# Kernel tuning notes

Hardware: AMD Instinct MI355X
Metric: run time of the kernel (lower is better)

Reference implementation:

```python
import jax, jax.numpy as jnp
import numpy as np

N_NODES = 100000
N_EDGES = 3200000


def sage_conv(x, src, dst, Wl, bl, Wr, n_nodes):
    # PyG SAGEConv: out = lin_l(mean_{j in N(i)} x_j) + lin_r(x_i)
    msgs = x[src]                                            # [E, d]
    agg = jax.ops.segment_sum(msgs, dst, num_segments=n_nodes)
    cnt = jax.ops.segment_sum(jnp.ones((src.shape[0],), x.dtype), dst,
                              num_segments=n_nodes)
    mean = agg / jnp.maximum(cnt, 1.0)[:, None]
    return mean @ Wl.T + bl + x @ Wr.T


def setup_inputs() -> dict:
    key = jax.random.key(0)
    ks = jax.random.split(key, 9)
    x = jax.random.normal(ks[0], (N_NODES, 6), dtype=jnp.float32)
    edge_index = jax.random.randint(ks[1], (2, N_EDGES), 0, N_NODES, dtype=jnp.int32)
    def glorot(k, shape):
        fan_in = shape[1]
        return jax.random.normal(k, shape, dtype=jnp.float32) / np.sqrt(fan_in)
    return {
        "x": x,
        "edge_index": edge_index,
        "W1l": glorot(ks[2], (12, 6)), "b1": jnp.zeros((12,), jnp.float32),
        "W1r": glorot(ks[3], (12, 6)),
        "W2l": glorot(ks[4], (24, 12)), "b2": jnp.zeros((24,), jnp.float32),
        "W2r": glorot(ks[5], (24, 12)),
        "W3l": glorot(ks[6], (6, 24)), "b3": jnp.zeros((6,), jnp.float32),
        "W3r": glorot(ks[7], (6, 24)),
    }


def reference(x, edge_index, W1l, b1, W1r, W2l, b2, W2r, W3l, b3, W3r):
    src, dst = edge_index[0], edge_index[1]
    h = jax.nn.relu(sage_conv(x, src, dst, W1l, b1, W1r, N_NODES))
    h = jax.nn.relu(sage_conv(h, src, dst, W2l, b2, W2r, N_NODES))
    z = sage_conv(h, src, dst, W3l, b3, W3r, N_NODES)          # [N, 6] encoding
    return z
```

## Files before the change

### kernel.cpp

```cpp
#include <hip/hip_runtime.h>
#include <hip/hip_fp16.h>


#define BSHIFT 9
#define BMASK  511
#define NBMAX  256
#define PART_EDGES 4096
#define BCAP   18000

#define NTL(p) __builtin_nontemporal_load(p)

__device__ __forceinline__ unsigned h2u(__half2 h) { return *reinterpret_cast<unsigned*>(&h); }
__device__ __forceinline__ __half2 u2h(unsigned u) { return *reinterpret_cast<__half2*>(&u); }

__device__ __forceinline__ __half2 red32(__half2 v) {
    int x;
    x = __builtin_amdgcn_update_dpp(0, (int)h2u(v), 0x128, 0xf, 0xf, true);
    v = __hadd2(v, u2h((unsigned)x));
    x = __builtin_amdgcn_update_dpp(0, (int)h2u(v), 0x124, 0xf, 0xf, true);
    v = __hadd2(v, u2h((unsigned)x));
    x = __builtin_amdgcn_update_dpp(0, (int)h2u(v), 0x122, 0xf, 0xf, true);
    v = __hadd2(v, u2h((unsigned)x));
    x = __builtin_amdgcn_update_dpp(0, (int)h2u(v), 0x121, 0xf, 0xf, true);
    v = __hadd2(v, u2h((unsigned)x));
    v = __hadd2(v, u2h(__shfl_xor(h2u(v), 16, 64)));
    return v;
}

__global__ void init_bcur(int* __restrict__ bcur, int nb) {
    int t = threadIdx.x;
    if (t < nb) bcur[t] = t * BCAP;
}

__global__ void __launch_bounds__(256)
partition_kernel(const int* __restrict__ src, const int* __restrict__ dst,
                 int* __restrict__ bcur, unsigned* __restrict__ pairs,
                 int E, int nb) {
    __shared__ int hcnt[NBMAX];
    __shared__ int hbase[NBMAX];
    __shared__ int lofs[NBMAX];
    __shared__ int ssc[256];
    __shared__ unsigned sorted[PART_EDGES];
    __shared__ int gpos[PART_EDGES];

    int lo = blockIdx.x * PART_EDGES;
    int hi = min(E, lo + PART_EDGES);
    int cnt = hi - lo;
    int t = threadIdx.x;

    for (int i = t; i < NBMAX; i += 256) hcnt[i] = 0;
    __syncthreads();

    int myd[16]; unsigned mys[16];
#pragma unroll
    for (int k = 0; k < 16; k++) {
        int i = lo + t + k * 256;
        if (i < hi) { myd[k] = NTL(dst + i); mys[k] = (unsigned)NTL(src + i); }
        else myd[k] = -1;
    }
#pragma unroll
    for (int k = 0; k < 16; k++)
        if (myd[k] >= 0) atomicAdd(&hcnt[myd[k] >> BSHIFT], 1);
    __syncthreads();

    int c = (t < nb) ? hcnt[t] : 0;
    if (t < nb) hbase[t] = c ? atomicAdd(&bcur[t], c) : 0;
    ssc[t] = c;
    __syncthreads();
    for (int off = 1; off < 256; off <<= 1) {
        int x = (t >= off) ? ssc[t - off] : 0;
        __syncthreads();
        ssc[t] += x;
        __syncthreads();
    }
    if (t < nb) { lofs[t] = ssc[t] - c; hcnt[t] = ssc[t] - c; }
    __syncthreads();

#pragma unroll
    for (int k = 0; k < 16; k++) {
        if (myd[k] >= 0) {
            int d = myd[k];
            int b = d >> BSHIFT;
            int r = atomicAdd(&hcnt[b], 1);
            sorted[r] = (mys[k] << BSHIFT) | (unsigned)(d & BMASK);
            gpos[r] = hbase[b] + (r - lofs[b]);
        }
    }
    __syncthreads();

    for (int i = t; i < cnt; i += 256)
        pairs[gpos[i]] = sorted[i];
}

__global__ void __launch_bounds__(1024)
csr_build(const unsigned* __restrict__ pairs,
          const int* __restrict__ bcur,
          int* __restrict__ deg, int* __restrict__ offsets,
          int* __restrict__ ssrc, int n) {
    __shared__ int ldeg[512];
    __shared__ int lcur[512];
    __shared__ int ssc[512];
    int b = blockIdx.x;
    int base = b * BCAP;
    int cnt = bcur[b] - base;
    int t = threadIdx.x;
    if (t < 512) ldeg[t] = 0;
    __syncthreads();
    for (int i = t; i < cnt; i += 1024)
        atomicAdd(&ldeg[NTL(pairs + base + i) & BMASK], 1);
    __syncthreads();
    if (t < 512) ssc[t] = ldeg[t];
    __syncthreads();
    for (int off = 1; off < 512; off <<= 1) {
        int x = (t >= off && t < 512) ? ssc[t - off] : 0;
        __syncthreads();
        if (t < 512) ssc[t] += x;
        __syncthreads();
    }
    if (t < 512) {
        int excl = ssc[t] - ldeg[t];
        lcur[t] = excl;
        int node = (b << BSHIFT) + t;
        if (node < n) { offsets[node] = base + excl; deg[node] = ldeg[t]; }
    }
    __syncthreads();
    for (int i = t; i < cnt; i += 1024) {
        unsigned p = NTL(pairs + base + i);
        int loc = p & BMASK;
        int pos = atomicAdd(&lcur[loc], 1);
        ssrc[base + pos] = (int)(p >> BSHIFT);
    }
}

__global__ void pack_x(const float* __restrict__ x, __half* __restrict__ xh,
                       __half* __restrict__ h1, int n) {
    int tid = blockIdx.x * blockDim.x + threadIdx.x;
    if (blockIdx.x == 0 && threadIdx.x < 16)
        h1[(size_t)n * 16 + threadIdx.x] = __float2half(0.f);
    if (tid >= n * 8) return;
    int i = tid >> 3, f = tid & 7;
    xh[tid] = __float2half((f < 6) ? x[i * 6 + f] : 0.f);
}

__global__ void __launch_bounds__(256)
sage_layer1(const __half* __restrict__ xh,
            const int* __restrict__ offsets,
            const int* __restrict__ deg,
            const int* __restrict__ ssrc,
            const float* __restrict__ Wl,
            const float* __restrict__ bb,
            const float* __restrict__ Wr,
            __half* __restrict__ h1, int n) {
    __shared__ float sWl[84], sWr[84], sb[12];
    int t = threadIdx.x;
    if (t < 72) { int r = t / 6, c = t % 6; sWl[r * 7 + c] = Wl[t]; sWr[r * 7 + c] = Wr[t]; }
    if (t < 12) sb[t] = bb[t];
    __syncthreads();

    int wid = (blockIdx.x * blockDim.x + threadIdx.x) >> 6;
    int nwaves = (gridDim.x * blockDim.x) >> 6;
    int wl = threadIdx.x & 63;
    int lane = wl & 31;
    int sub = wl >> 5;

    int r = (lane < 12) ? lane : 0;
    float wl_[6], wr_[6];
#pragma unroll
    for (int f = 0; f < 6; f++) { wl_[f] = sWl[r * 7 + f]; wr_[f] = sWr[r * 7 + f]; }
    float bias = sb[r];

    int npairs = (n + 1) >> 1;
    __half2 z2 = __float2half2_rn(0.f);
    for (int p = wid; p < npairs; p += nwaves) {
        int node = p * 2 + sub;
        bool valid = node < n;
        int off = valid ? offsets[node] : 0;
        int dg  = valid ? deg[node] : 0;

        __half2 acc[3] = { z2, z2, z2 };
        for (int e = lane; e < dg; e += 32) {
            int s = ssrc[off + e];
            uint4 r0 = *reinterpret_cast<const uint4*>(xh + (size_t)s * 8);
            acc[0] = __hadd2(acc[0], u2h(r0.x));
            acc[1] = __hadd2(acc[1], u2h(r0.y));
            acc[2] = __hadd2(acc[2], u2h(r0.z));
        }
#pragma unroll
        for (int k = 0; k < 3; k++) acc[k] = red32(acc[k]);

        if (valid && lane < 12) {
            float fa[6] = { __low2float(acc[0]), __high2float(acc[0]),
                            __low2float(acc[1]), __high2float(acc[1]),
                            __low2float(acc[2]), __high2float(acc[2]) };
            uint4 xr = *reinterpret_cast<const uint4*>(xh + (size_t)node * 8);
            float xi[6] = { __low2float(u2h(xr.x)), __high2float(u2h(xr.x)),
                            __low2float(u2h(xr.y)), __high2float(u2h(xr.y)),
                            __low2float(u2h(xr.z)), __high2float(u2h(xr.z)) };
            float inv = 1.f / (float)(dg > 0 ? dg : 1);
            float o = bias;
#pragma unroll
            for (int f = 0; f < 6; f++) o += fa[f] * inv * wl_[f] + xi[f] * wr_[f];
            h1[(size_t)node * 16 + lane] = __float2half(fmaxf(o, 0.f));
        }
    }
}

__global__ void __launch_bounds__(256)
sage_layer2(const __half* __restrict__ h1,
            const int* __restrict__ offsets,
            const int* __restrict__ deg,
            const int* __restrict__ ssrc,
            const float* __restrict__ W2l,
            const float* __restrict__ b2,
            const float* __restrict__ W2r,
            const float* __restrict__ W3l,
            const float* __restrict__ W3r,
            __half* __restrict__ z3lh,
            float* __restrict__ z3r, int n) {
    __shared__ float sW2l[312], sW2r[312], sW3[300], sb2[24];
    __shared__ __attribute__((aligned(16))) float sh2[4][48];
    int t = threadIdx.x;
    for (int i = t; i < 288; i += 256) {
        int r = i / 12, c = i % 12;
        sW2l[r * 13 + c] = W2l[i]; sW2r[r * 13 + c] = W2r[i];
    }
    if (t < 144) {
        int r = t / 24, c = t % 24;
        sW3[r * 25 + c] = W3l[t];
        sW3[(r + 6) * 25 + c] = W3r[t];
    }
    if (t < 24) sb2[t] = b2[t];
    __syncthreads();

    int wid = (blockIdx.x * blockDim.x + threadIdx.x) >> 6;
    int nwaves = (gridDim.x * blockDim.x) >> 6;
    int wv = threadIdx.x >> 6;
    int wl = threadIdx.x & 63;
    int lane = wl & 31;
    int sub = wl >> 5;

    int r2 = (lane < 24) ? lane : 0;
    float w2lr[12], w2rr[12];
#pragma unroll
    for (int f = 0; f < 12; f++) { w2lr[f] = sW2l[r2 * 13 + f]; w2rr[f] = sW2r[r2 * 13 + f]; }
    float bias = sb2[r2];
    int w3off = (lane < 12) ? lane * 25 : 0;
    float w3_[24];
#pragma unroll
    for (int o = 0; o < 24; o++) w3_[o] = sW3[w3off + o];

    int npairs = (n + 1) >> 1;
    __half2 z2 = __float2half2_rn(0.f);

    int p0 = wid, p1 = wid + nwaves;
    int node0 = 2 * p0 + sub, node1 = 2 * p1 + sub;
    bool v0 = (p0 < npairs) && (node0 < n);
    bool v1 = (p1 < npairs) && (node1 < n);
    int off0 = v0 ? offsets[node0] : 0, dg0 = v0 ? deg[node0] : 0;
    int off1 = v1 ? offsets[node1] : 0, dg1 = v1 ? deg[node1] : 0;

    __half2 a0[6], a1[6];
#pragma unroll
    for (int k = 0; k < 6; k++) { a0[k] = z2; a1[k] = z2; }
    int m = max(dg0, dg1);
    for (int e = lane; e < m; e += 32) {
        int q0 = ssrc[off0 + e];
        int q1 = ssrc[off1 + e];
        int s0 = (e < dg0) ? q0 : n;
        int s1 = (e < dg1) ? q1 : n;
        const char* rp0 = reinterpret_cast<const char*>(h1 + (size_t)s0 * 16);
        const char* rp1 = reinterpret_cast<const char*>(h1 + (size_t)s1 * 16);
        uint4 ra0 = *reinterpret_cast<const uint4*>(rp0);
        uint2 rb0 = *reinterpret_cast<const uint2*>(rp0 + 16);
        uint4 ra1 = *reinterpret_cast<const uint4*>(rp1);
        uint2 rb1 = *reinterpret_cast<const uint2*>(rp1 + 16);
        a0[0] = __hadd2(a0[0], u2h(ra0.x)); a0[1] = __hadd2(a0[1], u2h(ra0.y));
        a0[2] = __hadd2(a0[2], u2h(ra0.z)); a0[3] = __hadd2(a0[3], u2h(ra0.w));
        a0[4] = __hadd2(a0[4], u2h(rb0.x)); a0[5] = __hadd2(a0[5], u2h(rb0.y));
        a1[0] = __hadd2(a1[0], u2h(ra1.x)); a1[1] = __hadd2(a1[1], u2h(ra1.y));
        a1[2] = __hadd2(a1[2], u2h(ra1.z)); a1[3] = __hadd2(a1[3], u2h(ra1.w));
        a1[4] = __hadd2(a1[4], u2h(rb1.x)); a1[5] = __hadd2(a1[5], u2h(rb1.y));
    }

    auto finish = [&](int node, int dg, __half2* acc, bool valid) {
#pragma unroll
        for (int k = 0; k < 6; k++) acc[k] = red32(acc[k]);

        float h2v = 0.f;
        if (valid && lane < 24) {
            float fa[12];
#pragma unroll
            for (int k = 0; k < 6; k++) {
                fa[2 * k] = __low2float(acc[k]); fa[2 * k + 1] = __high2float(acc[k]);
            }
            const char* rp = reinterpret_cast<const char*>(h1 + (size_t)node * 16);
            uint4 x0 = *reinterpret_cast<const uint4*>(rp);
            uint2 x1 = *reinterpret_cast<const uint2*>(rp + 16);
            float xi[12] = { __low2float(u2h(x0.x)), __high2float(u2h(x0.x)),
                             __low2float(u2h(x0.y)), __high2float(u2h(x0.y)),
                             __low2float(u2h(x0.z)), __high2float(u2h(x0.z)),
                             __low2float(u2h(x0.w)), __high2float(u2h(x0.w)),
                             __low2float(u2h(x1.x)), __high2float(u2h(x1.x)),
                             __low2float(u2h(x1.y)), __high2float(u2h(x1.y)) };
            float inv = 1.f / (float)(dg > 0 ? dg : 1);
            float o = bias;
#pragma unroll
            for (int f = 0; f < 12; f++) o += fa[f] * inv * w2lr[f] + xi[f] * w2rr[f];
            h2v = fmaxf(o, 0.f);
        }
        if (lane < 24) sh2[wv][sub * 24 + lane] = h2v;
        float z = 0.f;
        if (lane < 12) {
            const float4* hp = reinterpret_cast<const float4*>(sh2[wv] + sub * 24);
#pragma unroll
            for (int k = 0; k < 6; k++) {
                float4 h4 = hp[k];
                z += h4.x * w3_[4 * k] + h4.y * w3_[4 * k + 1]
                   + h4.z * w3_[4 * k + 2] + h4.w * w3_[4 * k + 3];
            }
        }
        if (valid) {
            if (lane < 6)               z3lh[(size_t)node * 8 + lane] = __float2half(z);
            else if (lane < 8)          z3lh[(size_t)node * 8 + lane] = __float2half(0.f);
            if (lane >= 6 && lane < 12) z3r[(size_t)node * 6 + (lane - 6)] = z;
        }
    };
    finish(node0, dg0, a0, v0);
    finish(node1, dg1, a1, v1);
}

__global__ void __launch_bounds__(256)
sage_layer3(const __half* __restrict__ z3lh,
            const int* __restrict__ offsets,
            const int* __restrict__ deg,
            const int* __restrict__ ssrc,
            const float* __restrict__ b3,
            const float* __restrict__ z3r,
            float* __restrict__ out, int n) {
    int wid = (blockIdx.x * blockDim.x + threadIdx.x) >> 6;
    int nwaves = (gridDim.x * blockDim.x) >> 6;
    int wl = threadIdx.x & 63;
    int lane = wl & 31;
    int sub = wl >> 5;

    float b3v = b3[(lane < 6) ? lane : 0];

    int npairs = (n + 1) >> 1;
    __half2 z2 = __float2half2_rn(0.f);
    for (int p = wid; p < npairs; p += nwaves) {
        int node = p * 2 + sub;
        bool valid = node < n;
        int off = valid ? offsets[node] : 0;
        int dg  = valid ? deg[node] : 0;

        __half2 acc[3] = { z2, z2, z2 };
        for (int e = lane; e < dg; e += 32) {
            int s = ssrc[off + e];
            uint4 r0 = *reinterpret_cast<const uint4*>(z3lh + (size_t)s * 8);
            acc[0] = __hadd2(acc[0], u2h(r0.x));
            acc[1] = __hadd2(acc[1], u2h(r0.y));
            acc[2] = __hadd2(acc[2], u2h(r0.z));
        }
#pragma unroll
        for (int k = 0; k < 3; k++) acc[k] = red32(acc[k]);

        if (valid && lane < 6) {
            float fa[6] = { __low2float(acc[0]), __high2float(acc[0]),
                            __low2float(acc[1]), __high2float(acc[1]),
                            __low2float(acc[2]), __high2float(acc[2]) };
            float inv = 1.f / (float)(dg > 0 ? dg : 1);
            out[(size_t)node * 6 + lane] = fa[lane] * inv + b3v
                                         + z3r[(size_t)node * 6 + lane];
        }
    }
}

extern "C" void kernel_launch(void* const* d_in, const int* in_sizes, int n_in,
                              void* d_out, int out_size, void* d_ws, size_t ws_size,
                              hipStream_t stream) {
    const float* x   = (const float*)d_in[0];
    const int* eidx  = (const int*)d_in[1];
    const float* W1l = (const float*)d_in[2];
    const float* b1  = (const float*)d_in[3];
    const float* W1r = (const float*)d_in[4];
    const float* W2l = (const float*)d_in[5];
    const float* b2  = (const float*)d_in[6];
    const float* W2r = (const float*)d_in[7];
    const float* W3l = (const float*)d_in[8];
    const float* b3  = (const float*)d_in[9];
    const float* W3r = (const float*)d_in[10];

    const int n = in_sizes[0] / 6;
    const int E = in_sizes[1] / 2;
    const int* src = eidx;
    const int* dst = eidx + E;
    const int nb = (n + BMASK) >> BSHIFT;

    char* w = (char*)d_ws;
    auto carve = [&](size_t bytes) {
        char* p = w;
        w += (bytes + 255) & ~(size_t)255;
        return p;
    };
    int*      bcur    = (int*)carve((size_t)NBMAX * 4);
    unsigned* pairs   = (unsigned*)carve((size_t)nb * BCAP * 4);
    int*      ssrc    = (int*)carve((size_t)nb * BCAP * 4);
    int*      deg     = (int*)carve((size_t)n * 4);
    int*      offsets = (int*)carve((size_t)n * 4);
    __half*   xh      = (__half*)carve((size_t)n * 8 * 2);
    __half*   h1      = (__half*)carve((size_t)(n + 1) * 16 * 2);
    __half*   z3lh    = (__half*)carve((size_t)n * 8 * 2);
    float*    z3r     = (float*)carve((size_t)n * 6 * 4);

    const int part_blocks = (E + PART_EDGES - 1) / PART_EDGES;
    init_bcur<<<1, 256, 0, stream>>>(bcur, nb);
    partition_kernel<<<part_blocks, 256, 0, stream>>>(src, dst, bcur, pairs, E, nb);
    csr_build<<<nb, 1024, 0, stream>>>(pairs, bcur, deg, offsets, ssrc, n);
    pack_x<<<(n * 8 + 255) / 256, 256, 0, stream>>>(x, xh, h1, n);

    const int LBLK = 6250;
    sage_layer1<<<LBLK, 256, 0, stream>>>(xh, offsets, deg, ssrc, W1l, b1, W1r, h1, n);
    sage_layer2<<<LBLK, 256, 0, stream>>>(h1, offsets, deg, ssrc,
                                          W2l, b2, W2r, W3l, W3r, z3lh, z3r, n);
    sage_layer3<<<LBLK, 256, 0, stream>>>(z3lh, offsets, deg, ssrc, b3, z3r,
                                          (float*)d_out, n);
}
```

Baseline: 226.7 us.

## Merge init and pack kernels, unroll fixed node pairs, use half2 FMA for linear layers

The bcur-init kernel and the x-packing kernel become one prep kernel, which removes a launch. Layers 1 and 3 replace the grid-stride loop with two node pairs per wave, loading both pairs' offsets and degrees up front; this relies on the grid of 6250 blocks covering every pair in exactly two steps. The dense linear parts of layers 1 and 2 use packed half2 FMAs with fp16 weights instead of fp32 scalar math. That lowers precision and adds accumulation error in fp16.

```diff
diff --git a/kernel.cpp b/kernel.cpp
--- a/kernel.cpp
+++ b/kernel.cpp
@@ -27,9 +27,17 @@
     return v;
 }
 
-__global__ void init_bcur(int* __restrict__ bcur, int nb) {
-    int t = threadIdx.x;
-    if (t < nb) bcur[t] = t * BCAP;
+__global__ void __launch_bounds__(256)
+prep_kernel(const float* __restrict__ x, __half* __restrict__ xh,
+            __half* __restrict__ h1, int* __restrict__ bcur, int n, int nb) {
+    if (blockIdx.x == 0) {
+        if (threadIdx.x < nb) bcur[threadIdx.x] = threadIdx.x * BCAP;
+        if (threadIdx.x < 16) h1[(size_t)n * 16 + threadIdx.x] = __float2half(0.f);
+    }
+    int tid = blockIdx.x * blockDim.x + threadIdx.x;
+    if (tid >= n * 8) return;
+    int i = tid >> 3, f = tid & 7;
+    xh[tid] = __float2half((f < 6) ? x[i * 6 + f] : 0.f);
 }
 
 __global__ void __launch_bounds__(256)
@@ -132,16 +140,6 @@
     }
 }
 
-__global__ void pack_x(const float* __restrict__ x, __half* __restrict__ xh,
-                       __half* __restrict__ h1, int n) {
-    int tid = blockIdx.x * blockDim.x + threadIdx.x;
-    if (blockIdx.x == 0 && threadIdx.x < 16)
-        h1[(size_t)n * 16 + threadIdx.x] = __float2half(0.f);
-    if (tid >= n * 8) return;
-    int i = tid >> 3, f = tid & 7;
-    xh[tid] = __float2half((f < 6) ? x[i * 6 + f] : 0.f);
-}
-
 __global__ void __launch_bounds__(256)
 sage_layer1(const __half* __restrict__ xh,
             const int* __restrict__ offsets,
@@ -151,9 +149,16 @@
             const float* __restrict__ bb,
             const float* __restrict__ Wr,
             __half* __restrict__ h1, int n) {
-    __shared__ float sWl[84], sWr[84], sb[12];
+    __shared__ __half2 sWl2[36], sWr2[36];
+    __shared__ float sb[12];
     int t = threadIdx.x;
-    if (t < 72) { int r = t / 6, c = t % 6; sWl[r * 7 + c] = Wl[t]; sWr[r * 7 + c] = Wr[t]; }
+    if (t < 36) {
+        int r = t / 3, k = t % 3;
+        sWl2[t] = __halves2half2(__float2half(Wl[r * 6 + 2 * k]),
+                                 __float2half(Wl[r * 6 + 2 * k + 1]));
+        sWr2[t] = __halves2half2(__float2half(Wr[r * 6 + 2 * k]),
+                                 __float2half(Wr[r * 6 + 2 * k + 1]));
+    }
     if (t < 12) sb[t] = bb[t];
     __syncthreads();
 
@@ -164,19 +169,22 @@
     int sub = wl >> 5;
 
     int r = (lane < 12) ? lane : 0;
-    float wl_[6], wr_[6];
-#pragma unroll
-    for (int f = 0; f < 6; f++) { wl_[f] = sWl[r * 7 + f]; wr_[f] = sWr[r * 7 + f]; }
+    __half2 wl2[3], wr2[3];
+#pragma unroll
+    for (int k = 0; k < 3; k++) { wl2[k] = sWl2[r * 3 + k]; wr2[k] = sWr2[r * 3 + k]; }
     float bias = sb[r];
 
     int npairs = (n + 1) >> 1;
     __half2 z2 = __float2half2_rn(0.f);
-    for (int p = wid; p < npairs; p += nwaves) {
-        int node = p * 2 + sub;
-        bool valid = node < n;
-        int off = valid ? offsets[node] : 0;
-        int dg  = valid ? deg[node] : 0;
-
+
+    int pA = wid, pB = wid + nwaves;
+    int nodeA = 2 * pA + sub, nodeB = 2 * pB + sub;
+    bool vA = (pA < npairs) && (nodeA < n);
+    bool vB = (pB < npairs) && (nodeB < n);
+    int offA = vA ? offsets[nodeA] : 0, dgA = vA ? deg[nodeA] : 0;
+    int offB = vB ? offsets[nodeB] : 0, dgB = vB ? deg[nodeB] : 0;
+
+    auto do_pair = [&](int node, int off, int dg, bool valid) {
         __half2 acc[3] = { z2, z2, z2 };
         for (int e = lane; e < dg; e += 32) {
             int s = ssrc[off + e];
@@ -189,20 +197,22 @@
         for (int k = 0; k < 3; k++) acc[k] = red32(acc[k]);
 
         if (valid && lane < 12) {
-            float fa[6] = { __low2float(acc[0]), __high2float(acc[0]),
-                            __low2float(acc[1]), __high2float(acc[1]),
-                            __low2float(acc[2]), __high2float(acc[2]) };
             uint4 xr = *reinterpret_cast<const uint4*>(xh + (size_t)node * 8);
-            float xi[6] = { __low2float(u2h(xr.x)), __high2float(u2h(xr.x)),
-                            __low2float(u2h(xr.y)), __high2float(u2h(xr.y)),
-                            __low2float(u2h(xr.z)), __high2float(u2h(xr.z)) };
+            __half2 xi2[3] = { u2h(xr.x), u2h(xr.y), u2h(xr.z) };
+            __half2 S1 = z2, S2 = z2;
+#pragma unroll
+            for (int k = 0; k < 3; k++) {
+                S1 = __hfma2(acc[k], wl2[k], S1);
+                S2 = __hfma2(xi2[k], wr2[k], S2);
+            }
             float inv = 1.f / (float)(dg > 0 ? dg : 1);
-            float o = bias;
-#pragma unroll
-            for (int f = 0; f < 6; f++) o += fa[f] * inv * wl_[f] + xi[f] * wr_[f];
+            float o = (__low2float(S1) + __high2float(S1)) * inv
+                    + __low2float(S2) + __high2float(S2) + bias;
             h1[(size_t)node * 16 + lane] = __float2half(fmaxf(o, 0.f));
         }
-    }
+    };
+    do_pair(nodeA, offA, dgA, vA);
+    do_pair(nodeB, offB, dgB, vB);
 }
 
 __global__ void __launch_bounds__(256)
@@ -217,17 +227,19 @@
             const float* __restrict__ W3r,
             __half* __restrict__ z3lh,
             float* __restrict__ z3r, int n) {
-    __shared__ float sW2l[312], sW2r[312], sW3[300], sb2[24];
+    __shared__ __half2 sW2l2[144], sW2r2[144];
+    __shared__ float sW3[300], sb2[24];
     __shared__ __attribute__((aligned(16))) float sh2[4][48];
     int t = threadIdx.x;
-    for (int i = t; i < 288; i += 256) {
-        int r = i / 12, c = i % 12;
-        sW2l[r * 13 + c] = W2l[i]; sW2r[r * 13 + c] = W2r[i];
-    }
     if (t < 144) {
-        int r = t / 24, c = t % 24;
-        sW3[r * 25 + c] = W3l[t];
-        sW3[(r + 6) * 25 + c] = W3r[t];
+        int r = t / 6, k = t % 6;
+        sW2l2[t] = __halves2half2(__float2half(W2l[r * 12 + 2 * k]),
+                                  __float2half(W2l[r * 12 + 2 * k + 1]));
+        sW2r2[t] = __halves2half2(__float2half(W2r[r * 12 + 2 * k]),
+                                  __float2half(W2r[r * 12 + 2 * k + 1]));
+        int r3 = t / 24, c3 = t % 24;
+        sW3[r3 * 25 + c3] = W3l[t];
+        sW3[(r3 + 6) * 25 + c3] = W3r[t];
     }
     if (t < 24) sb2[t] = b2[t];
     __syncthreads();
@@ -240,9 +252,9 @@
     int sub = wl >> 5;
 
     int r2 = (lane < 24) ? lane : 0;
-    float w2lr[12], w2rr[12];
-#pragma unroll
-    for (int f = 0; f < 12; f++) { w2lr[f] = sW2l[r2 * 13 + f]; w2rr[f] = sW2r[r2 * 13 + f]; }
+    __half2 w2l2[6], w2r2[6];
+#pragma unroll
+    for (int k = 0; k < 6; k++) { w2l2[k] = sW2l2[r2 * 6 + k]; w2r2[k] = sW2r2[r2 * 6 + k]; }
     float bias = sb2[r2];
     int w3off = (lane < 12) ? lane * 25 : 0;
     float w3_[24];
@@ -288,24 +300,20 @@
 
         float h2v = 0.f;
         if (valid && lane < 24) {
-            float fa[12];
-#pragma unroll
-            for (int k = 0; k < 6; k++) {
-                fa[2 * k] = __low2float(acc[k]); fa[2 * k + 1] = __high2float(acc[k]);
-            }
             const char* rp = reinterpret_cast<const char*>(h1 + (size_t)node * 16);
             uint4 x0 = *reinterpret_cast<const uint4*>(rp);
             uint2 x1 = *reinterpret_cast<const uint2*>(rp + 16);
-            float xi[12] = { __low2float(u2h(x0.x)), __high2float(u2h(x0.x)),
-                             __low2float(u2h(x0.y)), __high2float(u2h(x0.y)),
-                             __low2float(u2h(x0.z)), __high2float(u2h(x0.z)),
-                             __low2float(u2h(x0.w)), __high2float(u2h(x0.w)),
-                             __low2float(u2h(x1.x)), __high2float(u2h(x1.x)),
-                             __low2float(u2h(x1.y)), __high2float(u2h(x1.y)) };
+            __half2 xi2[6] = { u2h(x0.x), u2h(x0.y), u2h(x0.z),
+                               u2h(x0.w), u2h(x1.x), u2h(x1.y) };
+            __half2 S1 = z2, S2 = z2;
+#pragma unroll
+            for (int k = 0; k < 6; k++) {
+                S1 = __hfma2(acc[k], w2l2[k], S1);
+                S2 = __hfma2(xi2[k], w2r2[k], S2);
+            }
             float inv = 1.f / (float)(dg > 0 ? dg : 1);
-            float o = bias;
-#pragma unroll
-            for (int f = 0; f < 12; f++) o += fa[f] * inv * w2lr[f] + xi[f] * w2rr[f];
+            float o = (__low2float(S1) + __high2float(S1)) * inv
+                    + __low2float(S2) + __high2float(S2) + bias;
             h2v = fmaxf(o, 0.f);
         }
         if (lane < 24) sh2[wv][sub * 24 + lane] = h2v;
@@ -347,12 +355,15 @@
 
     int npairs = (n + 1) >> 1;
     __half2 z2 = __float2half2_rn(0.f);
-    for (int p = wid; p < npairs; p += nwaves) {
-        int node = p * 2 + sub;
-        bool valid = node < n;
-        int off = valid ? offsets[node] : 0;
-        int dg  = valid ? deg[node] : 0;
-
+
+    int pA = wid, pB = wid + nwaves;
+    int nodeA = 2 * pA + sub, nodeB = 2 * pB + sub;
+    bool vA = (pA < npairs) && (nodeA < n);
+    bool vB = (pB < npairs) && (nodeB < n);
+    int offA = vA ? offsets[nodeA] : 0, dgA = vA ? deg[nodeA] : 0;
+    int offB = vB ? offsets[nodeB] : 0, dgB = vB ? deg[nodeB] : 0;
+
+    auto do_pair = [&](int node, int off, int dg, bool valid) {
         __half2 acc[3] = { z2, z2, z2 };
         for (int e = lane; e < dg; e += 32) {
             int s = ssrc[off + e];
@@ -372,7 +383,9 @@
             out[(size_t)node * 6 + lane] = fa[lane] * inv + b3v
                                          + z3r[(size_t)node * 6 + lane];
         }
-    }
+    };
+    do_pair(nodeA, offA, dgA, vA);
+    do_pair(nodeB, offB, dgB, vB);
 }
 
 extern "C" void kernel_launch(void* const* d_in, const int* in_sizes, int n_in,
@@ -413,10 +426,9 @@
     float*    z3r     = (float*)carve((size_t)n * 6 * 4);
 
     const int part_blocks = (E + PART_EDGES - 1) / PART_EDGES;
-    init_bcur<<<1, 256, 0, stream>>>(bcur, nb);
+    prep_kernel<<<(n * 8 + 255) / 256, 256, 0, stream>>>(x, xh, h1, bcur, n, nb);
     partition_kernel<<<part_blocks, 256, 0, stream>>>(src, dst, bcur, pairs, E, nb);
     csr_build<<<nb, 1024, 0, stream>>>(pairs, bcur, deg, offsets, ssrc, n);
-    pack_x<<<(n * 8 + 255) / 256, 256, 0, stream>>>(x, xh, h1, n);
 
     const int LBLK = 6250;
     sage_layer1<<<LBLK, 256, 0, stream>>>(xh, offsets, deg, ssrc, W1l, b1, W1r, h1, n);
```

Result: faster. 217.8 us (-3.9%).
